# Performance work log

Hardware: AMD Instinct MI355X
Metric: run time of the kernel (lower is better)

Reference implementation:

```python
import jax, jax.numpy as jnp
import numpy as np

M1 = M2 = M3 = 12   # Fourier modes kept per dim
WID = 32            # channel width
NL = 4              # number of Fourier layers
HID = 128           # skip-block hidden
INF = 9             # coord_dim + param_dim


def _gelu(x):
    return jax.nn.gelu(x, approximate=False)  # torch F.gelu default is exact erf


def _spectral_conv3d(x, w1, w2, w3, w4):
    # x: [B, Cin, S, V, T]; weights: [Cin, Cout, M1, M2, M3, 2]
    B, Ci, S, Vd, T = x.shape
    x_ft = jnp.fft.rfftn(x, axes=(-3, -2, -1))  # [B,Ci,S,V,T//2+1] complex64

    def cmul(sub, w):
        wc = w[..., 0] + 1j * w[..., 1]
        return jnp.einsum('bixyz,ioxyz->boxyz', sub, wc)

    Co = w1.shape[1]
    out_ft = jnp.zeros((B, Co, S, Vd, T // 2 + 1), dtype=x_ft.dtype)
    out_ft = out_ft.at[:, :, :M1, :M2, :M3].set(cmul(x_ft[:, :, :M1, :M2, :M3], w1))
    out_ft = out_ft.at[:, :, -M1:, :M2, :M3].set(cmul(x_ft[:, :, -M1:, :M2, :M3], w2))
    out_ft = out_ft.at[:, :, :M1, -M2:, :M3].set(cmul(x_ft[:, :, :M1, -M2:, :M3], w3))
    out_ft = out_ft.at[:, :, -M1:, -M2:, :M3].set(cmul(x_ft[:, :, -M1:, -M2:, :M3], w4))
    return jnp.fft.irfftn(out_ft, s=(S, Vd, T), axes=(-3, -2, -1))


def setup_inputs() -> dict:
    key = jax.random.key(0)
    ks = jax.random.split(key, 24)
    B, S, Vd, T = 4, 64, 64, 64
    scale = 1.0 / (WID * WID)
    spec_shape = (NL, WID, WID, M1, M2, M3, 2)
    inp = {
        'coords': jax.random.uniform(ks[0], (B, S, Vd, T, 3), dtype=jnp.float32),
        'params': jax.random.normal(ks[1], (B, 6), dtype=jnp.float32),
        'lift_w': 0.3 * jax.random.normal(ks[2], (INF, WID), dtype=jnp.float32),
        'lift_b': jnp.zeros((WID,), jnp.float32),
        'spec_w1': scale * jax.random.uniform(ks[3], spec_shape, dtype=jnp.float32),
        'spec_w2': scale * jax.random.uniform(ks[4], spec_shape, dtype=jnp.float32),
        'spec_w3': scale * jax.random.uniform(ks[5], spec_shape, dtype=jnp.float32),
        'spec_w4': scale * jax.random.uniform(ks[6], spec_shape, dtype=jnp.float32),
        'conv_w': 0.15 * jax.random.normal(ks[7], (NL, WID, WID), dtype=jnp.float32),
        'conv_b': jnp.zeros((NL, WID), jnp.float32),
        's1w': 0.3 * jax.random.normal(ks[8], (NL, INF, HID), dtype=jnp.float32),
        's1b': jnp.zeros((NL, HID), jnp.float32),
        's2w': 0.09 * jax.random.normal(ks[9], (NL, HID, HID), dtype=jnp.float32),
        's2b': jnp.zeros((NL, HID), jnp.float32),
        's3w': 0.09 * jax.random.normal(ks[10], (NL, HID, WID), dtype=jnp.float32),
        's3b': jnp.zeros((NL, WID), jnp.float32),
        'p1w': 0.15 * jax.random.normal(ks[11], (WID, WID // 2), dtype=jnp.float32),
        'p1b': jnp.zeros((WID // 2,), jnp.float32),
        'p2w': 0.25 * jax.random.normal(ks[12], (WID // 2, 1), dtype=jnp.float32),
        'p2b': jnp.zeros((1,), jnp.float32),
    }
    return inp


def reference(coords, params, lift_w, lift_b, spec_w1, spec_w2, spec_w3, spec_w4,
              conv_w, conv_b, s1w, s1b, s2w, s2b, s3w, s3b, p1w, p1b, p2w, p2b):
    B, S, Vd, T, _ = coords.shape
    # coordinate lift: broadcast params over grid, concat -> [B,S,V,T,9]
    pexp = jnp.broadcast_to(params[:, None, None, None, :], (B, S, Vd, T, params.shape[-1]))
    z = jnp.concatenate([coords, pexp], axis=-1)
    x = z @ lift_w + lift_b                      # [B,S,V,T,W]
    x = jnp.transpose(x, (0, 4, 1, 2, 3))        # [B,W,S,V,T]
    for i in range(NL):
        x1 = _spectral_conv3d(x, spec_w1[i], spec_w2[i], spec_w3[i], spec_w4[i])
        x2 = jnp.einsum('bixyz,oi->boxyz', x, conv_w[i]) + conv_b[i][None, :, None, None, None]
        xf = _gelu(x1 + x2)
        skip = _gelu(z @ s1w[i] + s1b[i])
        skip = _gelu(skip @ s2w[i] + s2b[i])
        skip = skip @ s3w[i] + s3b[i]            # [B,S,V,T,W]
        x = xf + jnp.transpose(skip, (0, 4, 1, 2, 3))
    x = jnp.transpose(x, (0, 2, 3, 4, 1))        # [B,S,V,T,W]
    h = _gelu(x @ p1w + p1b)
    out = (h @ p2w + p2b)[..., 0]                # [B,S,V,T]
    return out
```

## Files before the change

kernel.cpp:

```cpp
#include <hip/hip_runtime.h>
#include <hip/hip_bf16.h>
#include <math.h>

#define NB   4
#define NC   32
#define SVT  262144
#define VT   4096
#define NLAY 4
#define TWOPI_64 0.09817477042468103f

typedef __attribute__((ext_vector_type(8))) short bf16x8;
typedef __attribute__((ext_vector_type(4))) float f32x4;
typedef __attribute__((ext_vector_type(4))) unsigned short us4;

__device__ __forceinline__ float gelu_f(float x){
    float x2 = x * x;
    float u  = x * __builtin_fmaf(-0.10294322f, x2, -2.30220795f);
    float e  = __builtin_amdgcn_exp2f(u);
    return x * __builtin_amdgcn_rcpf(1.0f + e);
}

__device__ __forceinline__ unsigned short f2bf(float f){
    union { __hip_bfloat16 h; unsigned short u; } cv;
    cv.h = __float2bfloat16(f);
    return cv.u;
}
__device__ __forceinline__ float bf2f(unsigned short u){
    return __uint_as_float(((unsigned int)u) << 16);
}

__global__ __launch_bounds__(256) void k_prep(
    const float* __restrict__ params,
    const float* __restrict__ s1w, const float* __restrict__ s1b,
    const float* __restrict__ s2w, const float* __restrict__ s3w,
    const float* __restrict__ conv_w,
    unsigned short* __restrict__ w2bf,
    unsigned short* __restrict__ w3bf,
    unsigned short* __restrict__ tdft,
    unsigned short* __restrict__ T1h, unsigned short* __restrict__ T1l,
    unsigned short* __restrict__ T2h, unsigned short* __restrict__ T2l,
    float* __restrict__ pbq,
    unsigned short* __restrict__ w1dup,
    unsigned short* __restrict__ wcvh, unsigned short* __restrict__ wcvl)
{
    int g = blockIdx.x * 256 + threadIdx.x;
    if (g < 65536){
        int l = g >> 14, r = g & 16383;
        int c = r >> 7, k = r & 127;
        w2bf[g] = f2bf(s2w[l*16384 + k*128 + c]);
        return;
    }
    g -= 65536;
    if (g < 16384){
        int l = g >> 12, r = g & 4095;
        int c2 = r >> 7, k = r & 127;
        w3bf[g] = f2bf(s3w[l*4096 + k*32 + c2]);
        return;
    }
    g -= 16384;
    if (g < 2048){
        int o = g >> 6, t = g & 63;
        float val = 0.f;
        if (o < 24){
            int kz = o >> 1;
            float ang = (float)((kz * t) & 63) * TWOPI_64;
            float sn, cs; sincosf(ang, &sn, &cs);
            val = (o & 1) ? -sn : cs;
        }
        unsigned short h = f2bf(val);
        tdft[g]        = h;
        tdft[2048 + g] = f2bf(val - bf2f(h));
        return;
    }
    g -= 2048;
    if (g < 8192){
        int col = g >> 6, k1 = g & 63;
        int v = col >> 1, pout = col & 1;
        float val = 0.f;
        if (k1 < 48){
            int ky = k1 >> 1, pin = k1 & 1;
            int kya = (ky < 12) ? ky : ky + 40;
            float ang = (float)((kya * v) & 63) * TWOPI_64;
            float sn, cs; sincosf(ang, &sn, &cs);
            val = pout == 0 ? (pin == 0 ? cs : -sn) : (pin == 0 ? sn : cs);
        }
        unsigned short h = f2bf(val);
        T1h[g] = h;
        T1l[g] = f2bf(val - bf2f(h));
        return;
    }
    g -= 8192;
    if (g < 2048){
        int t = g >> 5, k2 = g & 31;
        float val = 0.f;
        if (k2 < 24){
            int kz = k2 >> 1, part = k2 & 1;
            float wk = (kz == 0) ? 1.f : 2.f;
            float ang = (float)((kz * t) & 63) * TWOPI_64;
            float sn, cs; sincosf(ang, &sn, &cs);
            val = (part ? -sn : cs) * wk * (1.f / 262144.f);
        }
        unsigned short h = f2bf(val);
        T2h[g] = h;
        T2l[g] = f2bf(val - bf2f(h));
        return;
    }
    g -= 2048;
    if (g < 2048){
        int l = g >> 9, b = (g >> 7) & 3, h = g & 127;
        float acc = s1b[l*128 + h];
        #pragma unroll
        for (int j = 0; j < 6; ++j)
            acc += params[b*6 + j] * bf2f(f2bf(s1w[l*1152 + (3 + j)*128 + h]));
        pbq[g] = acc;
        return;
    }
    g -= 2048;
    if (g < 4096){
        int l = g >> 10, rem = g & 1023;
        int h = rem >> 3, slot = rem & 7;
        float val = 0.f;
        if (slot != 3 && slot != 7){
            int row = (slot < 3) ? slot : slot - 4;
            val = bf2f(f2bf(s1w[l*1152 + row*128 + h]));
        }
        w1dup[g] = f2bf(val);
        return;
    }
    g -= 4096;
    if (g < 4096){
        float val = conv_w[g];
        unsigned short h = f2bf(val);
        wcvh[g] = h;
        wcvl[g] = f2bf(val - bf2f(h));
    }
}

__global__ __launch_bounds__(256) void k_lift(
    const float* __restrict__ coords, const float* __restrict__ params,
    const float* __restrict__ lw, const float* __restrict__ lb,
    float* __restrict__ x)
{
    size_t g = (size_t)blockIdx.x * 256 + threadIdx.x;
    int b = (int)(g >> 18);
    size_t p = g & (size_t)(SVT - 1);
    float z[9];
    z[0] = coords[g*3+0]; z[1] = coords[g*3+1]; z[2] = coords[g*3+2];
    #pragma unroll
    for (int j = 0; j < 6; ++j) z[3+j] = params[b*6+j];
    #pragma unroll
    for (int c = 0; c < 32; ++c){
        float acc = lb[c];
        #pragma unroll
        for (int j = 0; j < 9; ++j) acc += z[j] * lw[j*32 + c];
        x[(size_t)(b*32 + c) * SVT + p] = acc;
    }
}

__global__ __launch_bounds__(256) void k_fwdTV(
    const float* __restrict__ x, const unsigned short* __restrict__ tdft,
    float2* __restrict__ X2)
{
    __shared__ __align__(16) unsigned short Ahi[64][72], Alo[64][72];
    __shared__ __align__(16) unsigned short Bhi[32][72], Blo[32][72];
    __shared__ float2 a2[12][66];
    __shared__ float2 wtab[64];
    int tid = threadIdx.x;
    int bc = blockIdx.x >> 6;
    int s  = blockIdx.x & 63;
    if (tid < 64){
        float sn, cs;
        sincosf((float)tid * TWOPI_64, &sn, &cs);
        wtab[tid] = make_float2(cs, sn);
    }
    for (int i = tid; i < 2048; i += 256){
        int o = i >> 6, t = i & 63;
        Bhi[o][t] = tdft[i];
        Blo[o][t] = tdft[2048 + i];
    }
    {
        int row = tid >> 2, c0 = (tid & 3) << 4;
        const float* src = x + (size_t)bc * SVT + (size_t)s * VT + row*64 + c0;
        #pragma unroll
        for (int q = 0; q < 4; ++q){
            float4 v4 = *(const float4*)&src[q*4];
            float vv[4] = {v4.x, v4.y, v4.z, v4.w};
            #pragma unroll
            for (int e = 0; e < 4; ++e){
                unsigned short h = f2bf(vv[e]);
                Ahi[row][c0 + q*4 + e] = h;
                Alo[row][c0 + q*4 + e] = f2bf(vv[e] - bf2f(h));
            }
        }
    }
    __syncthreads();
    int l = tid & 63, w = tid >> 6;
    int lr = l & 15, kg = l >> 4;
    int r0 = w << 4;
    f32x4 acc[2];
    acc[0] = (f32x4){0.f,0.f,0.f,0.f}; acc[1] = (f32x4){0.f,0.f,0.f,0.f};
    #pragma unroll
    for (int kc = 0; kc < 2; ++kc){
        int ko = kc*32 + kg*8;
        bf16x8 ah = *(const bf16x8*)&Ahi[r0 + lr][ko];
        bf16x8 al = *(const bf16x8*)&Alo[r0 + lr][ko];
        #pragma unroll
        for (int n = 0; n < 2; ++n){
            bf16x8 bh = *(const bf16x8*)&Bhi[n*16 + lr][ko];
            bf16x8 bl = *(const bf16x8*)&Blo[n*16 + lr][ko];
            acc[n] = __builtin_amdgcn_mfma_f32_16x16x32_bf16(ah, bh, acc[n], 0, 0, 0);
            acc[n] = __builtin_amdgcn_mfma_f32_16x16x32_bf16(ah, bl, acc[n], 0, 0, 0);
            acc[n] = __builtin_amdgcn_mfma_f32_16x16x32_bf16(al, bh, acc[n], 0, 0, 0);
        }
    }
    #pragma unroll
    for (int n = 0; n < 2; ++n){
        int o = n*16 + lr;
        if (o < 24){
            int kz = o >> 1;
            #pragma unroll
            for (int r = 0; r < 4; ++r){
                int v = r0 + kg*4 + r;
                if (o & 1) a2[kz][v].y = acc[n][r];
                else       a2[kz][v].x = acc[n][r];
            }
        }
    }
    __syncthreads();
    for (int task = tid; task < 288; task += 256){
        int kz = task % 12;
        int ky = task / 12;
        int kya = (ky < 12) ? ky : ky + 40;
        float re = 0.f, im = 0.f;
        for (int v = 0; v < 64; ++v){
            float2 wv = wtab[(kya * v) & 63];
            float2 a  = a2[kz][v];
            re += a.x * wv.x + a.y * wv.y;
            im += a.y * wv.x - a.x * wv.y;
        }
        X2[((size_t)(bc*12 + kz) * 24 + ky) * 64 + s] = make_float2(re, im);
    }
}

__global__ __launch_bounds__(256) void k_fwdS(
    const float2* __restrict__ X2, float2* __restrict__ X3)
{
    __shared__ float2 cin[32][65];
    __shared__ float2 wtab[64];
    int tid = threadIdx.x;
    if (tid < 64){
        float sn, cs; sincosf((float)tid * TWOPI_64, &sn, &cs);
        wtab[tid] = make_float2(cs, sn);
    }
    int rbase = blockIdx.x * 32;
    for (int i = tid; i < 2048; i += 256){
        int row = i >> 6, s = i & 63;
        cin[row][s] = X2[(size_t)(rbase + row) * 64 + s];
    }
    __syncthreads();
    int row = tid & 31;
    int r = rbase + row;
    int kxg = tid >> 5;
    int kxs[3];
    #pragma unroll
    for (int j = 0; j < 3; ++j){ int kxi = kxg*3 + j; kxs[j] = (kxi < 12) ? kxi : kxi + 40; }
    float re[3] = {0,0,0}, im[3] = {0,0,0};
    for (int s = 0; s < 64; ++s){
        float2 cv = cin[row][s];
        #pragma unroll
        for (int j = 0; j < 3; ++j){
            float2 wv = wtab[(kxs[j] * s) & 63];
            re[j] += cv.x * wv.x + cv.y * wv.y;
            im[j] += cv.y * wv.x - cv.x * wv.y;
        }
    }
    int bc = r / 288; int kz = (r / 24) % 12; int ky = r % 24;
    #pragma unroll
    for (int j = 0; j < 3; ++j){
        int kxi = kxg*3 + j;
        X3[(size_t)bc * 6912 + (size_t)kxi * 288 + ky * 12 + kz] = make_float2(re[j], im[j]);
    }
}

__global__ __launch_bounds__(256) void k_modemix(
    const float2* __restrict__ X3,
    const float* __restrict__ w1, const float* __restrict__ w2,
    const float* __restrict__ w3, const float* __restrict__ w4,
    int layer, float2* __restrict__ Y)
{
    __shared__ float2 wlds[32][64];
    int tid = threadIdx.x;
    int m   = tid & 63;
    int b   = tid >> 6;
    int corner = blockIdx.y >> 3;
    int o0     = (blockIdx.y & 7) * 4;
    int moff0  = blockIdx.x * 64;
    const float* wsrc = (corner==0 ? w1 : corner==1 ? w2 : corner==2 ? w3 : w4)
                        + (size_t)layer * 3538944;
    int moff = moff0 + m;
    int m1  = moff / 144;
    int rem = moff - m1 * 144;
    int kx  = m1 + ((corner == 1 || corner == 3) ? 12 : 0);
    int mode_g = kx * 288 + rem + ((corner >= 2) ? 144 : 0);

    float xr[32], xi[32];
    const float2* xp = X3 + (size_t)b * 32 * 6912 + mode_g;
    #pragma unroll
    for (int i = 0; i < 32; ++i){
        float2 a = xp[(size_t)i * 6912];
        xr[i] = a.x; xi[i] = a.y;
    }
    for (int oo = 0; oo < 4; ++oo){
        int o = o0 + oo;
        __syncthreads();
        for (int j = tid; j < 2048; j += 256){
            int i = j >> 6, mm = j & 63;
            wlds[i][mm] = *(const float2*)&wsrc[((size_t)(i*32 + o) * 1728 + moff0 + mm) * 2];
        }
        __syncthreads();
        float re = 0.f, im = 0.f;
        #pragma unroll
        for (int i = 0; i < 32; ++i){
            float2 wv = wlds[i][m];
            re += xr[i]*wv.x - xi[i]*wv.y;
            im += xr[i]*wv.y + xi[i]*wv.x;
        }
        Y[(size_t)(b*32 + o) * 6912 + mode_g] = make_float2(re, im);
    }
}

__global__ __launch_bounds__(256) void k_invS(
    const float2* __restrict__ Y, float2* __restrict__ Z1)
{
    __shared__ float2 yin[24][24];
    __shared__ float2 wtab[64];
    int tid = threadIdx.x;
    if (tid < 64){
        float sn, cs; sincosf((float)tid * TWOPI_64, &sn, &cs);
        wtab[tid] = make_float2(cs, sn);
    }
    int bo = blockIdx.x / 12;
    int kz = blockIdx.x % 12;
    for (int i = tid; i < 576; i += 256){
        int kx = i / 24, ky = i % 24;
        yin[kx][ky] = Y[(size_t)bo * 6912 + (size_t)kx * 288 + ky * 12 + kz];
    }
    __syncthreads();
    int s = tid & 63;
    int kyg = tid >> 6;
    float re[6] = {0,0,0,0,0,0}, im[6] = {0,0,0,0,0,0};
    for (int kxi = 0; kxi < 24; ++kxi){
        int kxa = (kxi < 12) ? kxi : kxi + 40;
        float2 wv = wtab[(kxa * s) & 63];
        #pragma unroll
        for (int j = 0; j < 6; ++j){
            float2 a = yin[kxi][kyg*6 + j];
            re[j] += a.x * wv.x - a.y * wv.y;
            im[j] += a.x * wv.y + a.y * wv.x;
        }
    }
    #pragma unroll
    for (int j = 0; j < 6; ++j){
        int ky = kyg*6 + j;
        Z1[((size_t)(bo*12 + kz) * 64 + s) * 24 + ky] = make_float2(re[j], im[j]);
    }
}

__global__ __launch_bounds__(256) void k_cinvVT(
    const float* __restrict__ xin, const float2* __restrict__ Z1,
    const unsigned short* __restrict__ T2h, const unsigned short* __restrict__ T2l,
    const unsigned short* __restrict__ wcvh, const unsigned short* __restrict__ wcvl,
    const float* __restrict__ cb, int layer, float* __restrict__ xout)
{
    __shared__ __align__(16) unsigned short XT[2][256][40];
    __shared__ __align__(16) unsigned short A2h[128][40], A2l[128][40];
    __shared__ float2 wtab[64];
    int tid = threadIdx.x;
    int vg = blockIdx.x & 15;
    int s  = (blockIdx.x >> 4) & 63;
    int b  = blockIdx.x >> 10;
    if (tid < 64){
        float sn, cs; sincosf((float)tid * TWOPI_64, &sn, &cs);
        wtab[tid] = make_float2(cs, sn);
    }
    {
        int row = tid >> 1, half = tid & 1;
        us4 z = (us4){0,0,0,0};
        *(us4*)&A2h[row][24 + half*4] = z;
        *(us4*)&A2l[row][24 + half*4] = z;
    }
    {
        const float* xp = xin + (size_t)b*32*SVT + (size_t)s*VT + (size_t)vg*256 + tid;
        #pragma unroll
        for (int q = 0; q < 4; ++q){
            bf16x8 ph, pl;
            #pragma unroll
            for (int e = 0; e < 8; ++e){
                float v = xp[(size_t)(q*8 + e) * SVT];
                unsigned short h = f2bf(v);
                ph[e] = (short)h;
                pl[e] = (short)f2bf(v - bf2f(h));
            }
            *(bf16x8*)&XT[0][tid][q*8] = ph;
            *(bf16x8*)&XT[1][tid][q*8] = pl;
        }
    }
    __syncthreads();
    #pragma unroll
    for (int j = 0; j < 6; ++j){
        int task = tid + j*256;
        int o = task / 48, rem = task % 48;
        int kz = rem >> 2, vloc = rem & 3;
        int v = vg*4 + vloc;
        const float2* zp = Z1 + ((size_t)((b*32 + o)*12 + kz) * 64 + s) * 24;
        float re = 0.f, im = 0.f;
        #pragma unroll
        for (int ky = 0; ky < 24; ++ky){
            int kya = (ky < 12) ? ky : ky + 40;
            float2 wv = wtab[(kya * v) & 63];
            float2 a = zp[ky];
            re += a.x * wv.x - a.y * wv.y;
            im += a.x * wv.y + a.y * wv.x;
        }
        int row = o*4 + vloc;
        unsigned short hr = f2bf(re), hm = f2bf(im);
        A2h[row][2*kz  ] = hr; A2l[row][2*kz  ] = f2bf(re - bf2f(hr));
        A2h[row][2*kz+1] = hm; A2l[row][2*kz+1] = f2bf(im - bf2f(hm));
    }
    __syncthreads();
    int l = tid & 63, w = tid >> 6, lr = l & 15, kg = l >> 4;
    f32x4 dcv[2][4];
    #pragma unroll
    for (int ot = 0; ot < 2; ++ot){
        bf16x8 ah = *(const bf16x8*)&wcvh[layer*1024 + (ot*16 + lr)*32 + kg*8];
        bf16x8 al = *(const bf16x8*)&wcvl[layer*1024 + (ot*16 + lr)*32 + kg*8];
        #pragma unroll
        for (int ptt = 0; ptt < 4; ++ptt){
            bf16x8 bh = *(const bf16x8*)&XT[0][w*64 + ptt*16 + lr][kg*8];
            bf16x8 bl = *(const bf16x8*)&XT[1][w*64 + ptt*16 + lr][kg*8];
            f32x4 d = (f32x4){0.f,0.f,0.f,0.f};
            d = __builtin_amdgcn_mfma_f32_16x16x32_bf16(ah, bh, d, 0, 0, 0);
            d = __builtin_amdgcn_mfma_f32_16x16x32_bf16(ah, bl, d, 0, 0, 0);
            d = __builtin_amdgcn_mfma_f32_16x16x32_bf16(al, bh, d, 0, 0, 0);
            dcv[ot][ptt] = d;
        }
    }
    __syncthreads();
    float* x2s = (float*)&XT[0][0][0];
    #pragma unroll
    for (int ot = 0; ot < 2; ++ot)
        #pragma unroll
        for (int ptt = 0; ptt < 4; ++ptt)
            #pragma unroll
            for (int r = 0; r < 4; ++r)
                x2s[(ot*16 + kg*4 + r)*266 + w*64 + ptt*16 + lr] = dcv[ot][ptt][r];
    f32x4 dt[2][4];
    #pragma unroll
    for (int rt = 0; rt < 2; ++rt){
        bf16x8 ah = *(const bf16x8*)&A2h[w*32 + rt*16 + lr][kg*8];
        bf16x8 al = *(const bf16x8*)&A2l[w*32 + rt*16 + lr][kg*8];
        #pragma unroll
        for (int n = 0; n < 4; ++n){
            bf16x8 bh = *(const bf16x8*)&T2h[(n*16 + lr)*32 + kg*8];
            bf16x8 bl = *(const bf16x8*)&T2l[(n*16 + lr)*32 + kg*8];
            f32x4 d = (f32x4){0.f,0.f,0.f,0.f};
            d = __builtin_amdgcn_mfma_f32_16x16x32_bf16(ah, bh, d, 0, 0, 0);
            d = __builtin_amdgcn_mfma_f32_16x16x32_bf16(ah, bl, d, 0, 0, 0);
            d = __builtin_amdgcn_mfma_f32_16x16x32_bf16(al, bh, d, 0, 0, 0);
            dt[rt][n] = d;
        }
    }
    __syncthreads();
    size_t outb = (size_t)b*32*SVT + (size_t)s*VT + (size_t)vg*256;
    #pragma unroll
    for (int rt = 0; rt < 2; ++rt){
        int o = 8*w + rt*4 + kg;
        float cbv = cb[layer*32 + o];
        #pragma unroll
        for (int n = 0; n < 4; ++n){
            #pragma unroll
            for (int r = 0; r < 4; ++r){
                int pt = r*64 + n*16 + lr;
                float val = dt[rt][n][r] + x2s[o*266 + pt] + cbv;
                xout[outb + (size_t)o*SVT + pt] = gelu_f(val);
            }
        }
    }
}

template<int LAST>
__global__ __launch_bounds__(256, 8) void k_skip(
    const float* __restrict__ coords,
    const unsigned short* __restrict__ w1dup, const float* __restrict__ pbq,
    const unsigned short* __restrict__ w2bf, const float* __restrict__ s2b,
    const unsigned short* __restrict__ w3bf, const float* __restrict__ s3b,
    int layer, float* __restrict__ xio,
    const float* __restrict__ p1w, const float* __restrict__ p1b,
    const float* __restrict__ p2w, const float* __restrict__ p2b,
    float* __restrict__ out)
{
    __shared__ __align__(16) unsigned short A1[64][136];
    __shared__ __align__(16) unsigned short zst[4][16][8];

    int tid = threadIdx.x;
    size_t g0 = (size_t)blockIdx.x * 64;
    int b = (int)(g0 >> 18);
    const unsigned short* w2g = w2bf + (size_t)layer * 16384;
    const unsigned short* w3g = w3bf + (size_t)layer * 4096;
    const unsigned short* w1g = w1dup + (size_t)layer * 1024;
    const float* pbg = pbq + layer*512 + b*128;
    const float* b2g = s2b + layer*128;

    int l  = tid & 63;
    int w  = tid >> 6;
    int lr = l & 15;
    int kg = l >> 4;

    if (l < 16){
        size_t g = g0 + (size_t)w*16 + l;
        float z0 = coords[g*3+0], z1 = coords[g*3+1], z2 = coords[g*3+2];
        unsigned short h0 = f2bf(z0), h1 = f2bf(z1), h2 = f2bf(z2);
        bf16x8 pk;
        pk[0] = (short)h0; pk[1] = (short)h1; pk[2] = (short)h2; pk[3] = 0;
        pk[4] = (short)f2bf(z0 - bf2f(h0));
        pk[5] = (short)f2bf(z1 - bf2f(h1));
        pk[6] = (short)f2bf(z2 - bf2f(h2));
        pk[7] = 0;
        *(bf16x8*)&zst[w][l][0] = pk;
    }
    bf16x8 bz;
    if (kg == 0) bz = *(const bf16x8*)&zst[w][lr][0];
    else         bz = (bf16x8){0,0,0,0,0,0,0,0};

    {
        f32x4 accB[8];
        #pragma unroll
        for (int m = 0; m < 8; ++m) accB[m] = (f32x4){0.f,0.f,0.f,0.f};
        #pragma unroll
        for (int m = 0; m < 8; ++m){
            bf16x8 af = *(const bf16x8*)&w1g[(m*16 + lr)*8];
            accB[m] = __builtin_amdgcn_mfma_f32_16x16x32_bf16(af, bz, accB[m], 0, 0, 0);
        }
        #pragma unroll
        for (int m = 0; m < 8; ++m){
            int c0 = m*16 + kg*4;
            float4 bb = *(const float4*)&pbg[c0];
            us4 pk4;
            pk4[0] = f2bf(gelu_f(accB[m][0] + bb.x));
            pk4[1] = f2bf(gelu_f(accB[m][1] + bb.y));
            pk4[2] = f2bf(gelu_f(accB[m][2] + bb.z));
            pk4[3] = f2bf(gelu_f(accB[m][3] + bb.w));
            *(us4*)&A1[w*16 + lr][c0] = pk4;
        }
    }
    __syncthreads();

    f32x4 accC[2][4];
    #pragma unroll
    for (int mi = 0; mi < 2; ++mi)
        #pragma unroll
        for (int pt = 0; pt < 4; ++pt) accC[mi][pt] = (f32x4){0.f,0.f,0.f,0.f};
    #pragma unroll
    for (int kc = 0; kc < 4; ++kc){
        int ko = kc*32 + kg*8;
        bf16x8 a0 = *(const bf16x8*)&w2g[((2*w    )*16 + lr)*128 + ko];
        bf16x8 a1 = *(const bf16x8*)&w2g[((2*w + 1)*16 + lr)*128 + ko];
        #pragma unroll
        for (int pt = 0; pt < 4; ++pt){
            bf16x8 bb = *(const bf16x8*)&A1[pt*16 + lr][ko];
            accC[0][pt] = __builtin_amdgcn_mfma_f32_16x16x32_bf16(a0, bb, accC[0][pt], 0, 0, 0);
            accC[1][pt] = __builtin_amdgcn_mfma_f32_16x16x32_bf16(a1, bb, accC[1][pt], 0, 0, 0);
        }
    }
    __syncthreads();
    #pragma unroll
    for (int mi = 0; mi < 2; ++mi)
        #pragma unroll
        for (int pt = 0; pt < 4; ++pt){
            int c0 = (2*w + mi)*16 + kg*4;
            float4 bb = *(const float4*)&b2g[c0];
            us4 pk4;
            pk4[0] = f2bf(gelu_f(accC[mi][pt][0] + bb.x));
            pk4[1] = f2bf(gelu_f(accC[mi][pt][1] + bb.y));
            pk4[2] = f2bf(gelu_f(accC[mi][pt][2] + bb.z));
            pk4[3] = f2bf(gelu_f(accC[mi][pt][3] + bb.w));
            *(us4*)&A1[pt*16 + lr][c0] = pk4;
        }
    __syncthreads();

    int nD  = w & 1;
    int pt0 = (w >> 1) * 2;
    float b3v = s3b[layer*32 + nD*16 + lr];
    f32x4 c3[2];
    c3[0] = (f32x4){0.f,0.f,0.f,0.f}; c3[1] = (f32x4){0.f,0.f,0.f,0.f};
    #pragma unroll
    for (int kc = 0; kc < 4; ++kc){
        int ko = kc*32 + kg*8;
        bf16x8 bw3 = *(const bf16x8*)&w3g[(nD*16 + lr)*128 + ko];
        bf16x8 aa0 = *(const bf16x8*)&A1[(pt0    )*16 + lr][ko];
        bf16x8 aa1 = *(const bf16x8*)&A1[(pt0 + 1)*16 + lr][ko];
        c3[0] = __builtin_amdgcn_mfma_f32_16x16x32_bf16(aa0, bw3, c3[0], 0, 0, 0);
        c3[1] = __builtin_amdgcn_mfma_f32_16x16x32_bf16(aa1, bw3, c3[1], 0, 0, 0);
    }
    __syncthreads();

    float* outsT = (float*)&A1[0][0];
    {
        int c2 = nD*16 + lr;
        #pragma unroll
        for (int q = 0; q < 2; ++q){
            int p0 = (pt0 + q)*16 + kg*4;
            float4 v4;
            v4.x = c3[q][0] + b3v; v4.y = c3[q][1] + b3v;
            v4.z = c3[q][2] + b3v; v4.w = c3[q][3] + b3v;
            *(float4*)&outsT[c2*68 + p0] = v4;
        }
    }
    float* hs   = outsT + 2176;
    float* p1wS = outsT + 3264;
    float* smB  = outsT + 3776;
    if (LAST){
        for (int i = tid; i < 512; i += 256) p1wS[i] = p1w[i];
        if (tid < 16){ smB[tid] = p1b[tid]; smB[16 + tid] = p2w[tid]; }
        if (tid == 32) smB[32] = p2b[0];
    }
    __syncthreads();

    {
        int c  = tid >> 3;
        int pg = tid & 7;
        size_t prel = (g0 & (size_t)(SVT - 1)) + (size_t)pg*8;
        float* gp = xio + (((size_t)(b*32 + c)) << 18) + prel;
        float* op = &outsT[c*68 + pg*8];
        #pragma unroll
        for (int i = 0; i < 8; i += 4){
            float4 xv = *(const float4*)&gp[i];
            float4 ov = *(const float4*)&op[i];
            ov.x += xv.x; ov.y += xv.y; ov.z += xv.z; ov.w += xv.w;
            if (LAST) *(float4*)&op[i] = ov;
            else      *(float4*)&gp[i] = ov;
        }
    }
    if (LAST){
        __syncthreads();
        {
            int p  = tid & 63;
            int jq = tid >> 6;
            float h[4];
            #pragma unroll
            for (int j = 0; j < 4; ++j) h[j] = smB[jq*4 + j];
            for (int c = 0; c < 32; ++c){
                float xv = outsT[c*68 + p];
                #pragma unroll
                for (int j = 0; j < 4; ++j) h[j] += xv * p1wS[c*16 + jq*4 + j];
            }
            #pragma unroll
            for (int j = 0; j < 4; ++j) hs[p*17 + jq*4 + j] = h[j];
        }
        __syncthreads();
        if (tid < 64){
            float acc = smB[32];
            #pragma unroll
            for (int j = 0; j < 16; ++j) acc += gelu_f(hs[tid*17 + j]) * smB[16 + j];
            out[g0 + tid] = acc;
        }
    }
}

extern "C" void kernel_launch(void* const* d_in, const int* in_sizes, int n_in,
                              void* d_out, int out_size, void* d_ws, size_t ws_size,
                              hipStream_t stream)
{
    (void)in_sizes; (void)n_in; (void)out_size; (void)ws_size;
    const float* coords = (const float*)d_in[0];
    const float* params = (const float*)d_in[1];
    const float* lift_w = (const float*)d_in[2];
    const float* lift_b = (const float*)d_in[3];
    const float* sw1    = (const float*)d_in[4];
    const float* sw2    = (const float*)d_in[5];
    const float* sw3    = (const float*)d_in[6];
    const float* sw4    = (const float*)d_in[7];
    const float* conv_w = (const float*)d_in[8];
    const float* conv_b = (const float*)d_in[9];
    const float* s1w    = (const float*)d_in[10];
    const float* s1b    = (const float*)d_in[11];
    const float* s2w    = (const float*)d_in[12];
    const float* s2b    = (const float*)d_in[13];
    const float* s3w    = (const float*)d_in[14];
    const float* s3b    = (const float*)d_in[15];
    const float* p1w    = (const float*)d_in[16];
    const float* p1b    = (const float*)d_in[17];
    const float* p2w    = (const float*)d_in[18];
    const float* p2b    = (const float*)d_in[19];
    float* out = (float*)d_out;

    char* ws = (char*)d_ws;
    float*  xA = (float*)(ws);
    float2* X2 = (float2*)(ws + 134217728ull);
    float2* X3 = (float2*)(ws + 153092096ull);
    float2* Yb = (float2*)(ws + 160169984ull);
    unsigned short* w2bf  = (unsigned short*)(ws + 167247872ull);
    unsigned short* w3bf  = (unsigned short*)(ws + 167378944ull);
    unsigned short* tdft  = (unsigned short*)(ws + 167411712ull);
    unsigned short* T1h   = (unsigned short*)(ws + 167419904ull);
    unsigned short* T1l   = (unsigned short*)(ws + 167436288ull);
    unsigned short* T2h   = (unsigned short*)(ws + 167452672ull);
    unsigned short* T2l   = (unsigned short*)(ws + 167456768ull);
    float*          pbq   = (float*)(ws + 167460864ull);
    unsigned short* w1dup = (unsigned short*)(ws + 167469056ull);
    unsigned short* wcvh  = (unsigned short*)(ws + 167477248ull);
    unsigned short* wcvl  = (unsigned short*)(ws + 167485440ull);

    k_prep<<<408, 256, 0, stream>>>(params, s1w, s1b, s2w, s3w, conv_w,
                                    w2bf, w3bf, tdft, T1h, T1l, T2h, T2l,
                                    pbq, w1dup, wcvh, wcvl);
    k_lift<<<4096, 256, 0, stream>>>(coords, params, lift_w, lift_b, xA);

    for (int l = 0; l < NLAY; ++l){
        k_fwdTV<<<8192, 256, 0, stream>>>(xA, tdft, X2);
        k_fwdS<<<1152, 256, 0, stream>>>(X2, X3);
        dim3 gmm(27, 32);
        k_modemix<<<gmm, 256, 0, stream>>>(X3, sw1, sw2, sw3, sw4, l, Yb);
        k_invS<<<1536, 256, 0, stream>>>(Yb, X2);
        k_cinvVT<<<4096, 256, 0, stream>>>(xA, X2, T2h, T2l, wcvh, wcvl,
                                           conv_b, l, xA);
        if (l < NLAY - 1)
            k_skip<0><<<16384, 256, 0, stream>>>(coords, w1dup, pbq,
                w2bf, s2b, w3bf, s3b, l, xA, p1w, p1b, p2w, p2b, out);
        else
            k_skip<1><<<16384, 256, 0, stream>>>(coords, w1dup, pbq,
                w2bf, s2b, w3bf, s3b, l, xA, p1w, p1b, p2w, p2b, out);
    }
}
```

Baseline: 1.582 ms.

## Fuse inverse V/T transform with skip MLP into one kernel per layer

Merges k_cinvVT and k_skip into a single kernel handling 128 points per block. The activation xf stays in shared memory, so one global write and re-read of the full 32-channel field per layer is avoided. Tiles and shared-memory layout are reorganised, with padded rows and split 8-byte LDS loads, and launch bounds are lowered to 4 blocks per SM. The trade-off is larger shared-memory use and register pressure, which may reduce occupancy.

```diff
diff --git a/kernel.cpp b/kernel.cpp
--- a/kernel.cpp
+++ b/kernel.cpp
@@ -27,6 +27,15 @@
 }
 __device__ __forceinline__ float bf2f(unsigned short u){
     return __uint_as_float(((unsigned int)u) << 16);
+}
+
+__device__ __forceinline__ bf16x8 lds8(const unsigned short* p){
+    us4 a = *(const us4*)p;
+    us4 b = *(const us4*)(p + 4);
+    bf16x8 r;
+    r[0]=(short)a[0]; r[1]=(short)a[1]; r[2]=(short)a[2]; r[3]=(short)a[3];
+    r[4]=(short)b[0]; r[5]=(short)b[1]; r[6]=(short)b[2]; r[7]=(short)b[3];
+    return r;
 }
 
 __global__ __launch_bounds__(256) void k_prep(
@@ -366,52 +375,89 @@
     }
 }
 
-__global__ __launch_bounds__(256) void k_cinvVT(
+template<int LAST>
+__global__ __launch_bounds__(256, 4) void k_fused(
     const float* __restrict__ xin, const float2* __restrict__ Z1,
     const unsigned short* __restrict__ T2h, const unsigned short* __restrict__ T2l,
     const unsigned short* __restrict__ wcvh, const unsigned short* __restrict__ wcvl,
-    const float* __restrict__ cb, int layer, float* __restrict__ xout)
+    const float* __restrict__ cb, const float* __restrict__ coords,
+    const unsigned short* __restrict__ w1dup, const float* __restrict__ pbq,
+    const unsigned short* __restrict__ w2bf, const float* __restrict__ s2b,
+    const unsigned short* __restrict__ w3bf, const float* __restrict__ s3b,
+    int layer, float* __restrict__ xout,
+    const float* __restrict__ p1w, const float* __restrict__ p1b,
+    const float* __restrict__ p2w, const float* __restrict__ p2b,
+    float* __restrict__ out)
 {
-    __shared__ __align__(16) unsigned short XT[2][256][40];
-    __shared__ __align__(16) unsigned short A2h[128][40], A2l[128][40];
-    __shared__ float2 wtab[64];
+    __shared__ __align__(16) char LB[52736];
+    float2* wtab = (float2*)&LB[0];
+    unsigned short (*XTh)[36] = (unsigned short(*)[36])&LB[512];
+    unsigned short (*XTl)[36] = (unsigned short(*)[36])&LB[9728];
+    float* xf = (float*)&LB[512];
+    unsigned short (*A2h)[36] = (unsigned short(*)[36])&LB[18944];
+    unsigned short (*A2l)[36] = (unsigned short(*)[36])&LB[23552];
+    unsigned short (*A1)[132] = (unsigned short(*)[132])&LB[18944];
+    float* outsT = (float*)&LB[18944];
+    float* hs    = (float*)&LB[35840];
+    float* p1wS  = (float*)&LB[44544];
+    float* smB   = (float*)&LB[46592];
+
     int tid = threadIdx.x;
-    int vg = blockIdx.x & 15;
-    int s  = (blockIdx.x >> 4) & 63;
-    int b  = blockIdx.x >> 10;
+    int vp = blockIdx.x & 31;
+    int s  = (blockIdx.x >> 5) & 63;
+    int b  = blockIdx.x >> 11;
+    size_t base    = (size_t)b*32*SVT + (size_t)s*VT + (size_t)vp*128;
+    size_t gptbase = (size_t)b*SVT    + (size_t)s*VT + (size_t)vp*128;
+
+    const unsigned short* w2g = w2bf + (size_t)layer * 16384;
+    const unsigned short* w3g = w3bf + (size_t)layer * 4096;
+    const unsigned short* w1g = w1dup + (size_t)layer * 1024;
+    const float* pbg = pbq + layer*512 + b*128;
+    const float* b2g = s2b + layer*128;
+
     if (tid < 64){
         float sn, cs; sincosf((float)tid * TWOPI_64, &sn, &cs);
         wtab[tid] = make_float2(cs, sn);
     }
     {
-        int row = tid >> 1, half = tid & 1;
-        us4 z = (us4){0,0,0,0};
-        *(us4*)&A2h[row][24 + half*4] = z;
-        *(us4*)&A2l[row][24 + half*4] = z;
-    }
+        int pt = tid & 127, half = tid >> 7;
+        const float* xp = xin + base + pt;
+        #pragma unroll
+        for (int q = 0; q < 2; ++q){
+            int o0 = half*16 + q*8;
+            us4 pa, pb_, la, lb_;
+            #pragma unroll
+            for (int e = 0; e < 4; ++e){
+                float v = xp[(size_t)(o0 + e) * SVT];
+                unsigned short h = f2bf(v);
+                pa[e] = h; la[e] = f2bf(v - bf2f(h));
+            }
+            #pragma unroll
+            for (int e = 0; e < 4; ++e){
+                float v = xp[(size_t)(o0 + 4 + e) * SVT];
+                unsigned short h = f2bf(v);
+                pb_[e] = h; lb_[e] = f2bf(v - bf2f(h));
+            }
+            *(us4*)&XTh[pt][o0]     = pa;
+            *(us4*)&XTh[pt][o0 + 4] = pb_;
+            *(us4*)&XTl[pt][o0]     = la;
+            *(us4*)&XTl[pt][o0 + 4] = lb_;
+        }
+    }
+    __syncthreads();
     {
-        const float* xp = xin + (size_t)b*32*SVT + (size_t)s*VT + (size_t)vg*256 + tid;
-        #pragma unroll
-        for (int q = 0; q < 4; ++q){
-            bf16x8 ph, pl;
-            #pragma unroll
-            for (int e = 0; e < 8; ++e){
-                float v = xp[(size_t)(q*8 + e) * SVT];
-                unsigned short h = f2bf(v);
-                ph[e] = (short)h;
-                pl[e] = (short)f2bf(v - bf2f(h));
-            }
-            *(bf16x8*)&XT[0][tid][q*8] = ph;
-            *(bf16x8*)&XT[1][tid][q*8] = pl;
-        }
-    }
-    __syncthreads();
-    #pragma unroll
-    for (int j = 0; j < 6; ++j){
+        us4 z4 = (us4){0,0,0,0};
+        int t2 = tid & 127;
+        int row = t2 >> 1, g4 = t2 & 1;
+        if (tid < 128) *(us4*)&A2h[row][24 + g4*4] = z4;
+        else           *(us4*)&A2l[row][24 + g4*4] = z4;
+    }
+    #pragma unroll
+    for (int j = 0; j < 3; ++j){
         int task = tid + j*256;
-        int o = task / 48, rem = task % 48;
-        int kz = rem >> 2, vloc = rem & 3;
-        int v = vg*4 + vloc;
+        int row = task / 12, kz = task - row*12;
+        int vloc = row >> 5, o = row & 31;
+        int v = vp*2 + vloc;
         const float2* zp = Z1 + ((size_t)((b*32 + o)*12 + kz) * 64 + s) * 24;
         float re = 0.f, im = 0.f;
         #pragma unroll
@@ -422,117 +468,74 @@
             re += a.x * wv.x - a.y * wv.y;
             im += a.x * wv.y + a.y * wv.x;
         }
-        int row = o*4 + vloc;
         unsigned short hr = f2bf(re), hm = f2bf(im);
         A2h[row][2*kz  ] = hr; A2l[row][2*kz  ] = f2bf(re - bf2f(hr));
         A2h[row][2*kz+1] = hm; A2l[row][2*kz+1] = f2bf(im - bf2f(hm));
     }
     __syncthreads();
+
     int l = tid & 63, w = tid >> 6, lr = l & 15, kg = l >> 4;
-    f32x4 dcv[2][4];
-    #pragma unroll
-    for (int ot = 0; ot < 2; ++ot){
-        bf16x8 ah = *(const bf16x8*)&wcvh[layer*1024 + (ot*16 + lr)*32 + kg*8];
-        bf16x8 al = *(const bf16x8*)&wcvl[layer*1024 + (ot*16 + lr)*32 + kg*8];
+    int otile = w & 1, vloc_w = w >> 1;
+
+    f32x4 dcv[4], dt[4];
+    {
+        const unsigned short* wh = wcvh + layer*1024 + (otile*16 + lr)*32 + kg*8;
+        const unsigned short* wl = wcvl + layer*1024 + (otile*16 + lr)*32 + kg*8;
+        bf16x8 ah = *(const bf16x8*)wh;
+        bf16x8 al = *(const bf16x8*)wl;
         #pragma unroll
         for (int ptt = 0; ptt < 4; ++ptt){
-            bf16x8 bh = *(const bf16x8*)&XT[0][w*64 + ptt*16 + lr][kg*8];
-            bf16x8 bl = *(const bf16x8*)&XT[1][w*64 + ptt*16 + lr][kg*8];
+            int ptr_ = vloc_w*64 + ptt*16 + lr;
+            bf16x8 bh = lds8(&XTh[ptr_][kg*8]);
+            bf16x8 bl = lds8(&XTl[ptr_][kg*8]);
             f32x4 d = (f32x4){0.f,0.f,0.f,0.f};
             d = __builtin_amdgcn_mfma_f32_16x16x32_bf16(ah, bh, d, 0, 0, 0);
             d = __builtin_amdgcn_mfma_f32_16x16x32_bf16(ah, bl, d, 0, 0, 0);
             d = __builtin_amdgcn_mfma_f32_16x16x32_bf16(al, bh, d, 0, 0, 0);
-            dcv[ot][ptt] = d;
-        }
-    }
-    __syncthreads();
-    float* x2s = (float*)&XT[0][0][0];
-    #pragma unroll
-    for (int ot = 0; ot < 2; ++ot)
-        #pragma unroll
-        for (int ptt = 0; ptt < 4; ++ptt)
-            #pragma unroll
-            for (int r = 0; r < 4; ++r)
-                x2s[(ot*16 + kg*4 + r)*266 + w*64 + ptt*16 + lr] = dcv[ot][ptt][r];
-    f32x4 dt[2][4];
-    #pragma unroll
-    for (int rt = 0; rt < 2; ++rt){
-        bf16x8 ah = *(const bf16x8*)&A2h[w*32 + rt*16 + lr][kg*8];
-        bf16x8 al = *(const bf16x8*)&A2l[w*32 + rt*16 + lr][kg*8];
-        #pragma unroll
-        for (int n = 0; n < 4; ++n){
-            bf16x8 bh = *(const bf16x8*)&T2h[(n*16 + lr)*32 + kg*8];
-            bf16x8 bl = *(const bf16x8*)&T2l[(n*16 + lr)*32 + kg*8];
+            dcv[ptt] = d;
+        }
+    }
+    {
+        bf16x8 ah = lds8(&A2h[w*16 + lr][kg*8]);
+        bf16x8 al = lds8(&A2l[w*16 + lr][kg*8]);
+        #pragma unroll
+        for (int ptt = 0; ptt < 4; ++ptt){
+            bf16x8 bh = *(const bf16x8*)&T2h[(ptt*16 + lr)*32 + kg*8];
+            bf16x8 bl = *(const bf16x8*)&T2l[(ptt*16 + lr)*32 + kg*8];
             f32x4 d = (f32x4){0.f,0.f,0.f,0.f};
             d = __builtin_amdgcn_mfma_f32_16x16x32_bf16(ah, bh, d, 0, 0, 0);
             d = __builtin_amdgcn_mfma_f32_16x16x32_bf16(ah, bl, d, 0, 0, 0);
             d = __builtin_amdgcn_mfma_f32_16x16x32_bf16(al, bh, d, 0, 0, 0);
-            dt[rt][n] = d;
-        }
-    }
-    __syncthreads();
-    size_t outb = (size_t)b*32*SVT + (size_t)s*VT + (size_t)vg*256;
-    #pragma unroll
-    for (int rt = 0; rt < 2; ++rt){
-        int o = 8*w + rt*4 + kg;
-        float cbv = cb[layer*32 + o];
-        #pragma unroll
-        for (int n = 0; n < 4; ++n){
+            dt[ptt] = d;
+        }
+    }
+    __syncthreads();
+
+    {
+        float4 cbv = *(const float4*)&cb[layer*32 + otile*16 + kg*4];
+        float cbs[4] = {cbv.x, cbv.y, cbv.z, cbv.w};
+        #pragma unroll
+        for (int ptt = 0; ptt < 4; ++ptt){
+            int pt = vloc_w*64 + ptt*16 + lr;
             #pragma unroll
             for (int r = 0; r < 4; ++r){
-                int pt = r*64 + n*16 + lr;
-                float val = dt[rt][n][r] + x2s[o*266 + pt] + cbv;
-                xout[outb + (size_t)o*SVT + pt] = gelu_f(val);
+                int o = otile*16 + kg*4 + r;
+                xf[o*132 + pt] = gelu_f(dt[ptt][r] + dcv[ptt][r] + cbs[r]);
             }
         }
     }
-}
-
-template<int LAST>
-__global__ __launch_bounds__(256, 8) void k_skip(
-    const float* __restrict__ coords,
-    const unsigned short* __restrict__ w1dup, const float* __restrict__ pbq,
-    const unsigned short* __restrict__ w2bf, const float* __restrict__ s2b,
-    const unsigned short* __restrict__ w3bf, const float* __restrict__ s3b,
-    int layer, float* __restrict__ xio,
-    const float* __restrict__ p1w, const float* __restrict__ p1b,
-    const float* __restrict__ p2w, const float* __restrict__ p2b,
-    float* __restrict__ out)
-{
-    __shared__ __align__(16) unsigned short A1[64][136];
-    __shared__ __align__(16) unsigned short zst[4][16][8];
-
-    int tid = threadIdx.x;
-    size_t g0 = (size_t)blockIdx.x * 64;
-    int b = (int)(g0 >> 18);
-    const unsigned short* w2g = w2bf + (size_t)layer * 16384;
-    const unsigned short* w3g = w3bf + (size_t)layer * 4096;
-    const unsigned short* w1g = w1dup + (size_t)layer * 1024;
-    const float* pbg = pbq + layer*512 + b*128;
-    const float* b2g = s2b + layer*128;
-
-    int l  = tid & 63;
-    int w  = tid >> 6;
-    int lr = l & 15;
-    int kg = l >> 4;
-
-    if (l < 16){
-        size_t g = g0 + (size_t)w*16 + l;
-        float z0 = coords[g*3+0], z1 = coords[g*3+1], z2 = coords[g*3+2];
-        unsigned short h0 = f2bf(z0), h1 = f2bf(z1), h2 = f2bf(z2);
-        bf16x8 pk;
-        pk[0] = (short)h0; pk[1] = (short)h1; pk[2] = (short)h2; pk[3] = 0;
-        pk[4] = (short)f2bf(z0 - bf2f(h0));
-        pk[5] = (short)f2bf(z1 - bf2f(h1));
-        pk[6] = (short)f2bf(z2 - bf2f(h2));
-        pk[7] = 0;
-        *(bf16x8*)&zst[w][l][0] = pk;
-    }
-    bf16x8 bz;
-    if (kg == 0) bz = *(const bf16x8*)&zst[w][lr][0];
-    else         bz = (bf16x8){0,0,0,0,0,0,0,0};
-
-    {
+    #pragma unroll
+    for (int q = 0; q < 2; ++q){
+        bf16x8 bz = (bf16x8){0,0,0,0,0,0,0,0};
+        if (kg == 0){
+            size_t gp = gptbase + (size_t)w*32 + q*16 + lr;
+            float z0 = coords[gp*3+0], z1 = coords[gp*3+1], z2 = coords[gp*3+2];
+            unsigned short h0 = f2bf(z0), h1 = f2bf(z1), h2 = f2bf(z2);
+            bz[0] = (short)h0; bz[1] = (short)h1; bz[2] = (short)h2;
+            bz[4] = (short)f2bf(z0 - bf2f(h0));
+            bz[5] = (short)f2bf(z1 - bf2f(h1));
+            bz[6] = (short)f2bf(z2 - bf2f(h2));
+        }
         f32x4 accB[8];
         #pragma unroll
         for (int m = 0; m < 8; ++m) accB[m] = (f32x4){0.f,0.f,0.f,0.f};
@@ -550,75 +553,72 @@
             pk4[1] = f2bf(gelu_f(accB[m][1] + bb.y));
             pk4[2] = f2bf(gelu_f(accB[m][2] + bb.z));
             pk4[3] = f2bf(gelu_f(accB[m][3] + bb.w));
-            *(us4*)&A1[w*16 + lr][c0] = pk4;
-        }
-    }
-    __syncthreads();
-
-    f32x4 accC[2][4];
+            *(us4*)&A1[w*32 + q*16 + lr][c0] = pk4;
+        }
+    }
+    __syncthreads();
+
+    f32x4 accC[2][8];
     #pragma unroll
     for (int mi = 0; mi < 2; ++mi)
         #pragma unroll
-        for (int pt = 0; pt < 4; ++pt) accC[mi][pt] = (f32x4){0.f,0.f,0.f,0.f};
+        for (int ptt = 0; ptt < 8; ++ptt) accC[mi][ptt] = (f32x4){0.f,0.f,0.f,0.f};
     #pragma unroll
     for (int kc = 0; kc < 4; ++kc){
         int ko = kc*32 + kg*8;
         bf16x8 a0 = *(const bf16x8*)&w2g[((2*w    )*16 + lr)*128 + ko];
         bf16x8 a1 = *(const bf16x8*)&w2g[((2*w + 1)*16 + lr)*128 + ko];
         #pragma unroll
-        for (int pt = 0; pt < 4; ++pt){
-            bf16x8 bb = *(const bf16x8*)&A1[pt*16 + lr][ko];
-            accC[0][pt] = __builtin_amdgcn_mfma_f32_16x16x32_bf16(a0, bb, accC[0][pt], 0, 0, 0);
-            accC[1][pt] = __builtin_amdgcn_mfma_f32_16x16x32_bf16(a1, bb, accC[1][pt], 0, 0, 0);
+        for (int ptt = 0; ptt < 8; ++ptt){
+            bf16x8 bb = lds8(&A1[ptt*16 + lr][ko]);
+            accC[0][ptt] = __builtin_amdgcn_mfma_f32_16x16x32_bf16(a0, bb, accC[0][ptt], 0, 0, 0);
+            accC[1][ptt] = __builtin_amdgcn_mfma_f32_16x16x32_bf16(a1, bb, accC[1][ptt], 0, 0, 0);
         }
     }
     __syncthreads();
     #pragma unroll
     for (int mi = 0; mi < 2; ++mi)
         #pragma unroll
-        for (int pt = 0; pt < 4; ++pt){
+        for (int ptt = 0; ptt < 8; ++ptt){
             int c0 = (2*w + mi)*16 + kg*4;
             float4 bb = *(const float4*)&b2g[c0];
             us4 pk4;
-            pk4[0] = f2bf(gelu_f(accC[mi][pt][0] + bb.x));
-            pk4[1] = f2bf(gelu_f(accC[mi][pt][1] + bb.y));
-            pk4[2] = f2bf(gelu_f(accC[mi][pt][2] + bb.z));
-            pk4[3] = f2bf(gelu_f(accC[mi][pt][3] + bb.w));
-            *(us4*)&A1[pt*16 + lr][c0] = pk4;
+            pk4[0] = f2bf(gelu_f(accC[mi][ptt][0] + bb.x));
+            pk4[1] = f2bf(gelu_f(accC[mi][ptt][1] + bb.y));
+            pk4[2] = f2bf(gelu_f(accC[mi][ptt][2] + bb.z));
+            pk4[3] = f2bf(gelu_f(accC[mi][ptt][3] + bb.w));
+            *(us4*)&A1[ptt*16 + lr][c0] = pk4;
         }
     __syncthreads();
 
     int nD  = w & 1;
-    int pt0 = (w >> 1) * 2;
+    int pt0 = (w >> 1) * 4;
     float b3v = s3b[layer*32 + nD*16 + lr];
-    f32x4 c3[2];
-    c3[0] = (f32x4){0.f,0.f,0.f,0.f}; c3[1] = (f32x4){0.f,0.f,0.f,0.f};
+    f32x4 c3[4];
+    #pragma unroll
+    for (int q = 0; q < 4; ++q) c3[q] = (f32x4){0.f,0.f,0.f,0.f};
     #pragma unroll
     for (int kc = 0; kc < 4; ++kc){
         int ko = kc*32 + kg*8;
         bf16x8 bw3 = *(const bf16x8*)&w3g[(nD*16 + lr)*128 + ko];
-        bf16x8 aa0 = *(const bf16x8*)&A1[(pt0    )*16 + lr][ko];
-        bf16x8 aa1 = *(const bf16x8*)&A1[(pt0 + 1)*16 + lr][ko];
-        c3[0] = __builtin_amdgcn_mfma_f32_16x16x32_bf16(aa0, bw3, c3[0], 0, 0, 0);
-        c3[1] = __builtin_amdgcn_mfma_f32_16x16x32_bf16(aa1, bw3, c3[1], 0, 0, 0);
-    }
-    __syncthreads();
-
-    float* outsT = (float*)&A1[0][0];
+        #pragma unroll
+        for (int q = 0; q < 4; ++q){
+            bf16x8 aa = lds8(&A1[(pt0 + q)*16 + lr][ko]);
+            c3[q] = __builtin_amdgcn_mfma_f32_16x16x32_bf16(aa, bw3, c3[q], 0, 0, 0);
+        }
+    }
+    __syncthreads();
     {
         int c2 = nD*16 + lr;
         #pragma unroll
-        for (int q = 0; q < 2; ++q){
+        for (int q = 0; q < 4; ++q){
             int p0 = (pt0 + q)*16 + kg*4;
             float4 v4;
             v4.x = c3[q][0] + b3v; v4.y = c3[q][1] + b3v;
             v4.z = c3[q][2] + b3v; v4.w = c3[q][3] + b3v;
-            *(float4*)&outsT[c2*68 + p0] = v4;
-        }
-    }
-    float* hs   = outsT + 2176;
-    float* p1wS = outsT + 3264;
-    float* smB  = outsT + 3776;
+            *(float4*)&outsT[c2*132 + p0] = v4;
+        }
+    }
     if (LAST){
         for (int i = tid; i < 512; i += 256) p1wS[i] = p1w[i];
         if (tid < 16){ smB[tid] = p1b[tid]; smB[16 + tid] = p2w[tid]; }
@@ -629,40 +629,40 @@
     {
         int c  = tid >> 3;
         int pg = tid & 7;
-        size_t prel = (g0 & (size_t)(SVT - 1)) + (size_t)pg*8;
-        float* gp = xio + (((size_t)(b*32 + c)) << 18) + prel;
-        float* op = &outsT[c*68 + pg*8];
-        #pragma unroll
-        for (int i = 0; i < 8; i += 4){
-            float4 xv = *(const float4*)&gp[i];
-            float4 ov = *(const float4*)&op[i];
-            ov.x += xv.x; ov.y += xv.y; ov.z += xv.z; ov.w += xv.w;
-            if (LAST) *(float4*)&op[i] = ov;
-            else      *(float4*)&gp[i] = ov;
+        float* xfp = &xf[c*132 + pg*16];
+        float* otp = &outsT[c*132 + pg*16];
+        float* gp  = xout + base + (size_t)c*SVT + (size_t)pg*16;
+        #pragma unroll
+        for (int i = 0; i < 16; i += 4){
+            float4 sv = *(const float4*)&otp[i];
+            float4 xv = *(const float4*)&xfp[i];
+            sv.x += xv.x; sv.y += xv.y; sv.z += xv.z; sv.w += xv.w;
+            if (LAST) *(float4*)&otp[i] = sv;
+            else      *(float4*)&gp[i]  = sv;
         }
     }
     if (LAST){
         __syncthreads();
         {
-            int p  = tid & 63;
-            int jq = tid >> 6;
-            float h[4];
+            int p  = tid & 127;
+            int jq = tid >> 7;
+            float h[8];
             #pragma unroll
-            for (int j = 0; j < 4; ++j) h[j] = smB[jq*4 + j];
+            for (int j = 0; j < 8; ++j) h[j] = smB[jq*8 + j];
             for (int c = 0; c < 32; ++c){
-                float xv = outsT[c*68 + p];
+                float xv = outsT[c*132 + p];
                 #pragma unroll
-                for (int j = 0; j < 4; ++j) h[j] += xv * p1wS[c*16 + jq*4 + j];
+                for (int j = 0; j < 8; ++j) h[j] += xv * p1wS[c*16 + jq*8 + j];
             }
             #pragma unroll
-            for (int j = 0; j < 4; ++j) hs[p*17 + jq*4 + j] = h[j];
+            for (int j = 0; j < 8; ++j) hs[p*17 + jq*8 + j] = h[j];
         }
         __syncthreads();
-        if (tid < 64){
+        if (tid < 128){
             float acc = smB[32];
             #pragma unroll
             for (int j = 0; j < 16; ++j) acc += gelu_f(hs[tid*17 + j]) * smB[16 + j];
-            out[g0 + tid] = acc;
+            out[gptbase + tid] = acc;
         }
     }
 }
@@ -722,13 +722,13 @@
         dim3 gmm(27, 32);
         k_modemix<<<gmm, 256, 0, stream>>>(X3, sw1, sw2, sw3, sw4, l, Yb);
         k_invS<<<1536, 256, 0, stream>>>(Yb, X2);
-        k_cinvVT<<<4096, 256, 0, stream>>>(xA, X2, T2h, T2l, wcvh, wcvl,
-                                           conv_b, l, xA);
         if (l < NLAY - 1)
-            k_skip<0><<<16384, 256, 0, stream>>>(coords, w1dup, pbq,
-                w2bf, s2b, w3bf, s3b, l, xA, p1w, p1b, p2w, p2b, out);
+            k_fused<0><<<8192, 256, 0, stream>>>(xA, X2, T2h, T2l, wcvh, wcvl,
+                conv_b, coords, w1dup, pbq, w2bf, s2b, w3bf, s3b, l, xA,
+                p1w, p1b, p2w, p2b, out);
         else
-            k_skip<1><<<16384, 256, 0, stream>>>(coords, w1dup, pbq,
-                w2bf, s2b, w3bf, s3b, l, xA, p1w, p1b, p2w, p2b, out);
-    }
-}
+            k_fused<1><<<8192, 256, 0, stream>>>(xA, X2, T2h, T2l, wcvh, wcvl,
+                conv_b, coords, w1dup, pbq, w2bf, s2b, w3bf, s3b, l, xA,
+                p1w, p1b, p2w, p2b, out);
+    }
+}
```

Result: slower. 1.921 ms (+21.4%).

## Double skip-block tile to 128 points with 512 threads per block

Applied to the files above, without the earlier changes.

Grows the k_skip block to 512 threads covering 128 grid points. Each of the 8 waves now owns one 16-channel slice of the second hidden layer across all 8 point tiles, so every w2 weight fragment loaded is reused over more points. Shared-memory buffers, the transpose stride and the epilogue indexing are resized to match. The change also leaves several no-op leftover statements and a duplicate p1w load, and the larger shared-memory footprint per block may lower occupancy.

```diff
diff --git a/kernel.cpp b/kernel.cpp
--- a/kernel.cpp
+++ b/kernel.cpp
@@ -489,7 +489,7 @@
 }
 
 template<int LAST>
-__global__ __launch_bounds__(256, 8) void k_skip(
+__global__ __launch_bounds__(512, 8) void k_skip(
     const float* __restrict__ coords,
     const unsigned short* __restrict__ w1dup, const float* __restrict__ pbq,
     const unsigned short* __restrict__ w2bf, const float* __restrict__ s2b,
@@ -499,11 +499,11 @@
     const float* __restrict__ p2w, const float* __restrict__ p2b,
     float* __restrict__ out)
 {
-    __shared__ __align__(16) unsigned short A1[64][136];
-    __shared__ __align__(16) unsigned short zst[4][16][8];
+    __shared__ __align__(16) unsigned short A1[128][136];
+    __shared__ __align__(16) unsigned short zst[8][16][8];
 
     int tid = threadIdx.x;
-    size_t g0 = (size_t)blockIdx.x * 64;
+    size_t g0 = (size_t)blockIdx.x * 128;
     int b = (int)(g0 >> 18);
     const unsigned short* w2g = w2bf + (size_t)layer * 16384;
     const unsigned short* w3g = w3bf + (size_t)layer * 4096;
@@ -555,37 +555,33 @@
     }
     __syncthreads();
 
-    f32x4 accC[2][4];
-    #pragma unroll
-    for (int mi = 0; mi < 2; ++mi)
-        #pragma unroll
-        for (int pt = 0; pt < 4; ++pt) accC[mi][pt] = (f32x4){0.f,0.f,0.f,0.f};
+    f32x4 accC[8];
+    #pragma unroll
+    for (int pt = 0; pt < 8; ++pt) accC[pt] = (f32x4){0.f,0.f,0.f,0.f};
     #pragma unroll
     for (int kc = 0; kc < 4; ++kc){
         int ko = kc*32 + kg*8;
-        bf16x8 a0 = *(const bf16x8*)&w2g[((2*w    )*16 + lr)*128 + ko];
-        bf16x8 a1 = *(const bf16x8*)&w2g[((2*w + 1)*16 + lr)*128 + ko];
-        #pragma unroll
-        for (int pt = 0; pt < 4; ++pt){
+        bf16x8 a0 = *(const bf16x8*)&w2g[(w*16 + lr)*128 + ko];
+        #pragma unroll
+        for (int pt = 0; pt < 8; ++pt){
             bf16x8 bb = *(const bf16x8*)&A1[pt*16 + lr][ko];
-            accC[0][pt] = __builtin_amdgcn_mfma_f32_16x16x32_bf16(a0, bb, accC[0][pt], 0, 0, 0);
-            accC[1][pt] = __builtin_amdgcn_mfma_f32_16x16x32_bf16(a1, bb, accC[1][pt], 0, 0, 0);
-        }
-    }
-    __syncthreads();
-    #pragma unroll
-    for (int mi = 0; mi < 2; ++mi)
-        #pragma unroll
-        for (int pt = 0; pt < 4; ++pt){
-            int c0 = (2*w + mi)*16 + kg*4;
-            float4 bb = *(const float4*)&b2g[c0];
+            accC[pt] = __builtin_amdgcn_mfma_f32_16x16x32_bf16(a0, bb, accC[pt], 0, 0, 0);
+        }
+    }
+    __syncthreads();
+    {
+        int c0 = w*16 + kg*4;
+        float4 bb = *(const float4*)&b2g[c0];
+        #pragma unroll
+        for (int pt = 0; pt < 8; ++pt){
             us4 pk4;
-            pk4[0] = f2bf(gelu_f(accC[mi][pt][0] + bb.x));
-            pk4[1] = f2bf(gelu_f(accC[mi][pt][1] + bb.y));
-            pk4[2] = f2bf(gelu_f(accC[mi][pt][2] + bb.z));
-            pk4[3] = f2bf(gelu_f(accC[mi][pt][3] + bb.w));
+            pk4[0] = f2bf(gelu_f(accC[pt][0] + bb.x));
+            pk4[1] = f2bf(gelu_f(accC[pt][1] + bb.y));
+            pk4[2] = f2bf(gelu_f(accC[pt][2] + bb.z));
+            pk4[3] = f2bf(gelu_f(accC[pt][3] + bb.w));
             *(us4*)&A1[pt*16 + lr][c0] = pk4;
         }
+    }
     __syncthreads();
 
     int nD  = w & 1;
@@ -605,6 +601,9 @@
     __syncthreads();
 
     float* outsT = (float*)&A1[0][0];
+    float* hs    = outsT + 4224;
+    float* p1wS  = outsT + 6400;
+    float* smB   = outsT + 6912;
     {
         int c2 = nD*16 + lr;
         #pragma unroll
@@ -613,25 +612,26 @@
             float4 v4;
             v4.x = c3[q][0] + b3v; v4.y = c3[q][1] + b3v;
             v4.z = c3[q][2] + b3v; v4.w = c3[q][3] + b3v;
-            *(float4*)&outsT[c2*68 + p0] = v4;
-        }
-    }
-    float* hs   = outsT + 2176;
-    float* p1wS = outsT + 3264;
-    float* smB  = outsT + 3776;
+            *(float4*)&outsT[c2*132 + p0] = v4;
+        }
+    }
     if (LAST){
-        for (int i = tid; i < 512; i += 256) p1wS[i] = p1w[i];
+        for (int i = tid; i < 512; i += 512) p1wS[i] = p1w[i];
+        if (tid < 512) { if (tid < 512 && tid < 512) {} }
+        for (int i = tid; i < 512; i += 512) {}
         if (tid < 16){ smB[tid] = p1b[tid]; smB[16 + tid] = p2w[tid]; }
         if (tid == 32) smB[32] = p2b[0];
+        if (tid >= 64 && tid < 64+512-512) {}
+        if (tid < 512 && tid < 512) p1wS[tid] = p1w[tid];
     }
     __syncthreads();
 
     {
-        int c  = tid >> 3;
-        int pg = tid & 7;
+        int c  = tid >> 4;
+        int pg = tid & 15;
         size_t prel = (g0 & (size_t)(SVT - 1)) + (size_t)pg*8;
         float* gp = xio + (((size_t)(b*32 + c)) << 18) + prel;
-        float* op = &outsT[c*68 + pg*8];
+        float* op = &outsT[c*132 + pg*8];
         #pragma unroll
         for (int i = 0; i < 8; i += 4){
             float4 xv = *(const float4*)&gp[i];
@@ -644,13 +644,13 @@
     if (LAST){
         __syncthreads();
         {
-            int p  = tid & 63;
-            int jq = tid >> 6;
+            int p  = tid & 127;
+            int jq = tid >> 7;
             float h[4];
             #pragma unroll
             for (int j = 0; j < 4; ++j) h[j] = smB[jq*4 + j];
             for (int c = 0; c < 32; ++c){
-                float xv = outsT[c*68 + p];
+                float xv = outsT[c*132 + p];
                 #pragma unroll
                 for (int j = 0; j < 4; ++j) h[j] += xv * p1wS[c*16 + jq*4 + j];
             }
@@ -658,7 +658,7 @@
             for (int j = 0; j < 4; ++j) hs[p*17 + jq*4 + j] = h[j];
         }
         __syncthreads();
-        if (tid < 64){
+        if (tid < 128){
             float acc = smB[32];
             #pragma unroll
             for (int j = 0; j < 16; ++j) acc += gelu_f(hs[tid*17 + j]) * smB[16 + j];
@@ -725,10 +725,10 @@
         k_cinvVT<<<4096, 256, 0, stream>>>(xA, X2, T2h, T2l, wcvh, wcvl,
                                            conv_b, l, xA);
         if (l < NLAY - 1)
-            k_skip<0><<<16384, 256, 0, stream>>>(coords, w1dup, pbq,
+            k_skip<0><<<8192, 512, 0, stream>>>(coords, w1dup, pbq,
                 w2bf, s2b, w3bf, s3b, l, xA, p1w, p1b, p2w, p2b, out);
         else
-            k_skip<1><<<16384, 256, 0, stream>>>(coords, w1dup, pbq,
+            k_skip<1><<<8192, 512, 0, stream>>>(coords, w1dup, pbq,
                 w2bf, s2b, w3bf, s3b, l, xA, p1w, p1b, p2w, p2b, out);
     }
 }
```

After: 1.553 ms. Within noise of the previous version (-1.8%).
